# Optimization experiments

Hardware: AMD Instinct MI355X
Metric: run time of the kernel (lower is better)

## Reference

```python
import jax, jax.numpy as jnp
import numpy as np

N_NODES = 50000
N_EDGES = 1600000
IN_DIM = 256
OUT_DIM = 128
T = 8
V_THRESHOLD = 1.0
TAU = 2.0
STEP_SIZE = 0.1


def setup_inputs() -> dict:
    key = jax.random.key(0)
    k1, k2, k3 = jax.random.split(key, 3)
    x = jax.random.normal(k1, (N_NODES, IN_DIM), dtype=jnp.float32)
    W = jax.random.normal(k2, (IN_DIM, OUT_DIM), dtype=jnp.float32) / np.sqrt(IN_DIM)
    edge_index = jax.random.randint(k3, (2, N_EDGES), 0, N_NODES, dtype=jnp.int64)
    return {"x": x, "W": W, "edge_index": edge_index}


def gcn_conv(x, W, edge_index):
    # GCNConv (no bias): h = D^{-1/2} (A + I) D^{-1/2} (x @ W)
    n = x.shape[0]
    h = x @ W  # [N, OUT]
    loops = jnp.arange(n, dtype=edge_index.dtype)
    src = jnp.concatenate([edge_index[0], loops])
    dst = jnp.concatenate([edge_index[1], loops])
    deg = jax.ops.segment_sum(jnp.ones_like(dst, dtype=h.dtype), dst, num_segments=n)
    dinv = jnp.where(deg > 0, jax.lax.rsqrt(deg), 0.0)
    norm = dinv[src] * dinv[dst]  # [E+N]
    msgs = h[src] * norm[:, None]
    return jax.ops.segment_sum(msgs, dst, num_segments=n)  # [N, OUT]


def reference(x, W, edge_index):
    h = gcn_conv(x, W, edge_index)            # encoder output, [N, OUT]
    u = h * STEP_SIZE                          # per-step tangent input
    z0 = jnp.zeros_like(h)                     # manifold origin

    def step(z, _):
        # leaky charge toward input current, fire on threshold, soft reset
        Hm = z + (u - z) / TAU
        o = (Hm >= V_THRESHOLD).astype(Hm.dtype)
        z_new = Hm - o * V_THRESHOLD
        return z_new, (o, z_new)

    _, (o_seq, z_seq) = jax.lax.scan(step, z0, None, length=T)
    return o_seq, z_seq  # each [T, N, OUT]
```

## Files before the change

kernel.cpp:

```cpp
#include <hip/hip_runtime.h>
#include <hip/hip_bf16.h>

#define N_NODES 50000
#define N_EDGES 1600000
#define IN_DIM  256
#define OUT_DIM 128
#define T_STEPS 8
#define NREP    8

typedef __attribute__((ext_vector_type(8))) short bf16x8;
typedef __attribute__((ext_vector_type(4))) float f32x4;


__device__ inline unsigned short bf_hi_trunc(float x) {
    return (unsigned short)(__float_as_uint(x) >> 16);
}
__device__ inline float bf_to_f(unsigned short u) {
    return __uint_as_float((unsigned)u << 16);
}
__device__ inline unsigned short f2bf_rne(float a) {
    __hip_bfloat16 t = __float2bfloat16(a);
    return *(unsigned short*)&t;
}
__device__ inline float bf_lo(unsigned p) { return __uint_as_float(p << 16); }
__device__ inline float bf_hi(unsigned p) { return __uint_as_float(p & 0xffff0000u); }

__global__ __launch_bounds__(256) void
k_count(const float* __restrict__ W,
        unsigned short* __restrict__ Wt_hi,
        unsigned short* __restrict__ Wt_lo,
        const int* __restrict__ edge, int* __restrict__ cnt_x) {
    int idx = blockIdx.x * 256 + threadIdx.x;
    int* my = cnt_x + (blockIdx.x & (NREP - 1)) * N_NODES;
    if (idx < N_EDGES / 4) {
        int4 d = ((const int4*)(edge + N_EDGES))[idx];
        atomicAdd(&my[d.x], 1);
        atomicAdd(&my[d.y], 1);
        atomicAdd(&my[d.z], 1);
        atomicAdd(&my[d.w], 1);
    }
    if (idx < 32768) {
        int n = idx >> 8;
        int k = idx & 255;
        float w = W[k * OUT_DIM + n];
        unsigned short hi = bf_hi_trunc(w);
        Wt_hi[idx] = hi;
        Wt_lo[idx] = f2bf_rne(w - bf_to_f(hi));
    }
}

__global__ __launch_bounds__(256) void
k_scanA(const int* __restrict__ cnt_x, int* __restrict__ part) {
    int t = threadIdx.x;
    int i4 = blockIdx.x * 256 + t;
    int4 v = make_int4(0, 0, 0, 0);
    if (i4 < 12500) {
#pragma unroll
        for (int r = 0; r < NREP; ++r) {
            int4 c = ((const int4*)(cnt_x + r * N_NODES))[i4];
            v.x += c.x; v.y += c.y; v.z += c.z; v.w += c.w;
        }
    }
    int s = v.x + v.y + v.z + v.w;
    __shared__ int sd[256];
    sd[t] = s; __syncthreads();
    for (int o = 128; o > 0; o >>= 1) {
        if (t < o) sd[t] += sd[t + o];
        __syncthreads();
    }
    if (t == 0) part[blockIdx.x] = sd[0];
}

__global__ void k_scanB(int* __restrict__ part) {
    int l = threadIdx.x;
    int v = (l < 49) ? part[l] : 0;
    int orig = v;
    for (int o = 1; o < 64; o <<= 1) {
        int u = __shfl_up(v, o);
        if (l >= o) v += u;
    }
    if (l < 49) part[l] = v - orig;
}

__global__ __launch_bounds__(256) void
k_scanC(const int* __restrict__ cnt_x, const int* __restrict__ part,
        int* __restrict__ offs, int* __restrict__ deg,
        int* __restrict__ fill_x, float* __restrict__ dinv) {
    int t = threadIdx.x;
    int i4 = blockIdx.x * 256 + t;
    int4 vr[NREP];
    int4 tot = make_int4(0, 0, 0, 0);
    if (i4 < 12500) {
#pragma unroll
        for (int r = 0; r < NREP; ++r) {
            vr[r] = ((const int4*)(cnt_x + r * N_NODES))[i4];
            tot.x += vr[r].x; tot.y += vr[r].y;
            tot.z += vr[r].z; tot.w += vr[r].w;
        }
    } else {
#pragma unroll
        for (int r = 0; r < NREP; ++r) vr[r] = make_int4(0, 0, 0, 0);
    }
    int s = tot.x + tot.y + tot.z + tot.w;
    __shared__ int sd[256];
    sd[t] = s; __syncthreads();
    for (int o = 1; o < 256; o <<= 1) {
        int u = (t >= o) ? sd[t - o] : 0;
        __syncthreads();
        sd[t] += u;
        __syncthreads();
    }
    if (i4 < 12500) {
        int base = part[blockIdx.x] + sd[t] - s;
        int4 o4;
        o4.x = base;
        o4.y = o4.x + tot.x;
        o4.z = o4.y + tot.y;
        o4.w = o4.z + tot.z;
        ((int4*)offs)[i4] = o4;
        ((int4*)deg)[i4]  = tot;
        float4 d4;
        d4.x = rsqrtf((float)(tot.x + 1));
        d4.y = rsqrtf((float)(tot.y + 1));
        d4.z = rsqrtf((float)(tot.z + 1));
        d4.w = rsqrtf((float)(tot.w + 1));
        ((float4*)dinv)[i4] = d4;
        int c0 = o4.x, c1 = o4.y, c2 = o4.z, c3 = o4.w;
#pragma unroll
        for (int r = 0; r < NREP; ++r) {
            int4 c4 = make_int4(c0, c1, c2, c3);
            ((int4*)(fill_x + r * N_NODES))[i4] = c4;
            c0 += vr[r].x; c1 += vr[r].y; c2 += vr[r].z; c3 += vr[r].w;
        }
    }
}

__global__ __launch_bounds__(256) void
k_gemm(const float* __restrict__ x,
       const unsigned short* __restrict__ Wt_hi,
       const unsigned short* __restrict__ Wt_lo,
       const float* __restrict__ dinv,
       unsigned short* __restrict__ hs) {
    int wave = blockIdx.x * 4 + (threadIdx.x >> 6);
    if (wave >= N_NODES / 16) return;
    int lane = threadIdx.x & 63;
    int quad = lane >> 4;
    int r16  = lane & 15;
    int m0 = wave * 16;

    f32x4 acc[8];
#pragma unroll
    for (int nt = 0; nt < 8; ++nt) acc[nt] = (f32x4){0.f, 0.f, 0.f, 0.f};

#pragma unroll
    for (int kt = 0; kt < 8; ++kt) {
        int k0 = kt * 32 + quad * 8;
        const float* xp = x + (size_t)(m0 + r16) * IN_DIM + k0;
        float4 v0 = *(const float4*)xp;
        float4 v1 = *(const float4*)(xp + 4);
        float vv[8] = {v0.x, v0.y, v0.z, v0.w, v1.x, v1.y, v1.z, v1.w};
        union { bf16x8 v; unsigned short u[8]; } ahi, alo;
#pragma unroll
        for (int j = 0; j < 8; ++j) {
            unsigned short hi = bf_hi_trunc(vv[j]);
            ahi.u[j] = hi;
            alo.u[j] = f2bf_rne(vv[j] - bf_to_f(hi));
        }
#pragma unroll
        for (int nt = 0; nt < 8; ++nt) {
            size_t woff = (size_t)(nt * 16 + r16) * IN_DIM + k0;
            bf16x8 bhi = *(const bf16x8*)(Wt_hi + woff);
            bf16x8 blo = *(const bf16x8*)(Wt_lo + woff);
            acc[nt] = __builtin_amdgcn_mfma_f32_16x16x32_bf16(ahi.v, bhi, acc[nt], 0, 0, 0);
            acc[nt] = __builtin_amdgcn_mfma_f32_16x16x32_bf16(alo.v, bhi, acc[nt], 0, 0, 0);
            acc[nt] = __builtin_amdgcn_mfma_f32_16x16x32_bf16(ahi.v, blo, acc[nt], 0, 0, 0);
        }
    }
    float dr[4];
#pragma unroll
    for (int r = 0; r < 4; ++r) dr[r] = dinv[m0 + quad * 4 + r];
#pragma unroll
    for (int nt = 0; nt < 8; ++nt) {
#pragma unroll
        for (int r = 0; r < 4; ++r) {
            int row = m0 + quad * 4 + r;
            int col = nt * 16 + r16;
            hs[(size_t)row * OUT_DIM + col] = f2bf_rne(acc[nt][r] * dr[r]);
        }
    }
}

__global__ __launch_bounds__(256) void
k_fill(const int* __restrict__ edge, int* __restrict__ fill_x,
       unsigned short* __restrict__ csr) {
    int e4 = blockIdx.x * 256 + threadIdx.x;
    int* my = fill_x + (blockIdx.x & (NREP - 1)) * N_NODES;
    if (e4 < N_EDGES / 4) {
        int4 s = ((const int4*)edge)[e4];
        int4 d = ((const int4*)(edge + N_EDGES))[e4];
        int p;
        p = atomicAdd(&my[d.x], 1); csr[p] = (unsigned short)s.x;
        p = atomicAdd(&my[d.y], 1); csr[p] = (unsigned short)s.y;
        p = atomicAdd(&my[d.z], 1); csr[p] = (unsigned short)s.z;
        p = atomicAdd(&my[d.w], 1); csr[p] = (unsigned short)s.w;
    }
}

__global__ __launch_bounds__(256) void
k_agg_snn(const unsigned short* __restrict__ hs,
          const int* __restrict__ offs, const int* __restrict__ deg,
          const float* __restrict__ dinv,
          const unsigned short* __restrict__ csr,
          float* __restrict__ out) {
    int node = blockIdx.x * 4 + (threadIdx.x >> 6);
    int lane = threadIdx.x & 63;
    bool hi  = (lane >= 32);
    int  loff = (lane & 31) * 8;
    const char* hsb = (const char*)hs;

    uint2 qs = *(const uint2*)(hsb + (size_t)node * 256 + loff);
    float a0 = hi ? bf_lo(qs.x) : 0.f;
    float a1 = hi ? bf_hi(qs.x) : 0.f;
    float a2 = hi ? bf_lo(qs.y) : 0.f;
    float a3 = hi ? bf_hi(qs.y) : 0.f;

    int beg = __builtin_amdgcn_readfirstlane(offs[node]);
    int end = __builtin_amdgcn_readfirstlane(offs[node] + deg[node]);

    int j = beg;
    if (j & 1) {
        unsigned s = csr[j];
        if (!hi) {
            uint2 q = *(const uint2*)(hsb + (size_t)s * 256 + loff);
            a0 += bf_lo(q.x); a1 += bf_hi(q.x);
            a2 += bf_lo(q.y); a3 += bf_hi(q.y);
        }
        ++j;
    }
    int nd = (end - j) >> 1;
    const unsigned* cw = (const unsigned*)(csr + j);
    int k = 0;
    for (; k + 8 <= nd; k += 8) {
        unsigned d[8];
#pragma unroll
        for (int q = 0; q < 8; ++q) d[q] = cw[k + q];
        uint2 g[8];
#pragma unroll
        for (int q = 0; q < 8; ++q) {
            unsigned s = hi ? (d[q] >> 16) : (d[q] & 0xffffu);
            g[q] = *(const uint2*)(hsb + (size_t)s * 256 + loff);
        }
#pragma unroll
        for (int q = 0; q < 8; ++q) {
            a0 += bf_lo(g[q].x); a1 += bf_hi(g[q].x);
            a2 += bf_lo(g[q].y); a3 += bf_hi(g[q].y);
        }
    }
    for (; k < nd; ++k) {
        unsigned d = cw[k];
        unsigned s = hi ? (d >> 16) : (d & 0xffffu);
        uint2 q = *(const uint2*)(hsb + (size_t)s * 256 + loff);
        a0 += bf_lo(q.x); a1 += bf_hi(q.x);
        a2 += bf_lo(q.y); a3 += bf_hi(q.y);
    }
    int jt = j + 2 * nd;
    if (jt < end) {
        unsigned s = csr[jt];
        if (!hi) {
            uint2 q = *(const uint2*)(hsb + (size_t)s * 256 + loff);
            a0 += bf_lo(q.x); a1 += bf_hi(q.x);
            a2 += bf_lo(q.y); a3 += bf_hi(q.y);
        }
    }

    a0 += __shfl(a0, lane ^ 32);
    a1 += __shfl(a1, lane ^ 32);
    a2 += __shfl(a2, lane ^ 32);
    a3 += __shfl(a3, lane ^ 32);

    float di = dinv[node];
    float u0 = a0 * di * 0.1f, u1 = a1 * di * 0.1f;
    float u2 = a2 * di * 0.1f, u3 = a3 * di * 0.1f;
    float z0 = 0.f, z1 = 0.f, z2 = 0.f, z3 = 0.f;

    const size_t plane = (size_t)N_NODES * 128;
    size_t base = (size_t)node * 128 + (size_t)(lane & 31) * 4
                + (hi ? (size_t)T_STEPS * plane : 0);
#pragma unroll
    for (int t = 0; t < T_STEPS; ++t) {
        float H0 = z0 + (u0 - z0) * 0.5f;
        float H1 = z1 + (u1 - z1) * 0.5f;
        float H2 = z2 + (u2 - z2) * 0.5f;
        float H3 = z3 + (u3 - z3) * 0.5f;
        float o0 = (H0 >= 1.0f) ? 1.0f : 0.0f;
        float o1 = (H1 >= 1.0f) ? 1.0f : 0.0f;
        float o2 = (H2 >= 1.0f) ? 1.0f : 0.0f;
        float o3 = (H3 >= 1.0f) ? 1.0f : 0.0f;
        z0 = H0 - o0; z1 = H1 - o1; z2 = H2 - o2; z3 = H3 - o3;
        f32x4 v = {hi ? z0 : o0, hi ? z1 : o1,
                   hi ? z2 : o2, hi ? z3 : o3};
        __builtin_nontemporal_store(v, (f32x4*)(out + base + (size_t)t * plane));
    }
}

extern "C" void kernel_launch(void* const* d_in, const int* in_sizes, int n_in,
                              void* d_out, int out_size, void* d_ws, size_t ws_size,
                              hipStream_t stream) {
    const float* x  = (const float*)d_in[0];
    const float* W  = (const float*)d_in[1];
    const int*   ei = (const int*)d_in[2];
    float* out = (float*)d_out;

    char* ws = (char*)d_ws;
    unsigned short* hs     = (unsigned short*)(ws + 0);
    unsigned short* Wt_hi  = (unsigned short*)(ws + 12800000);
    unsigned short* Wt_lo  = (unsigned short*)(ws + 12865536);
    int*            cnt_x  = (int*)(ws + 12931072);
    int*            fill_x = (int*)(ws + 14531072);
    int*            offs   = (int*)(ws + 16131072);
    int*            deg    = (int*)(ws + 16331072);
    float*          dinv   = (float*)(ws + 16531072);
    int*            part   = (int*)(ws + 16731072);
    unsigned short* csr    = (unsigned short*)(ws + 16731328);

    hipMemsetAsync(cnt_x, 0, 1600000, stream);

    k_count<<<1563, 256, 0, stream>>>(W, Wt_hi, Wt_lo, ei, cnt_x);
    k_scanA<<<49, 256, 0, stream>>>(cnt_x, part);
    k_scanB<<<1, 64, 0, stream>>>(part);
    k_scanC<<<49, 256, 0, stream>>>(cnt_x, part, offs, deg, fill_x, dinv);
    k_gemm<<<782, 256, 0, stream>>>(x, Wt_hi, Wt_lo, dinv, hs);
    k_fill<<<1563, 256, 0, stream>>>(ei, fill_x, csr);
    k_agg_snn<<<12500, 256, 0, stream>>>(hs, offs, deg, dinv, csr, out);
}
```

Baseline: 694.3 us.

## Split hs into column slabs for cache-resident gathers and fuse gemm with fill

The GEMM output hs is stored as four column slabs of 32 features each, 3.2 MB per slab. The aggregation kernel runs four passes, one per slab, so each pass gathers from a slab small enough to stay in L2, and each wave handles four edges at once with 16 lanes per edge. The GEMM and CSR fill kernels are merged into one launch by block-index range, so the two independent workloads can overlap. In exchange, the CSR indices and the per-node offsets are re-read four times, each gather shrinks to 4 bytes, and output stores become narrower 8-byte writes.

```diff
diff --git a/kernel.cpp b/kernel.cpp
--- a/kernel.cpp
+++ b/kernel.cpp
@@ -10,6 +10,7 @@
 
 typedef __attribute__((ext_vector_type(8))) short bf16x8;
 typedef __attribute__((ext_vector_type(4))) float f32x4;
+typedef __attribute__((ext_vector_type(2))) float f32x2;
 
 
 __device__ inline unsigned short bf_hi_trunc(float x) {
@@ -128,178 +129,176 @@
         int c0 = o4.x, c1 = o4.y, c2 = o4.z, c3 = o4.w;
 #pragma unroll
         for (int r = 0; r < NREP; ++r) {
-            int4 c4 = make_int4(c0, c1, c2, c3);
-            ((int4*)(fill_x + r * N_NODES))[i4] = c4;
+            ((int4*)(fill_x + r * N_NODES))[i4] = make_int4(c0, c1, c2, c3);
             c0 += vr[r].x; c1 += vr[r].y; c2 += vr[r].z; c3 += vr[r].w;
         }
     }
 }
 
 __global__ __launch_bounds__(256) void
-k_gemm(const float* __restrict__ x,
-       const unsigned short* __restrict__ Wt_hi,
-       const unsigned short* __restrict__ Wt_lo,
-       const float* __restrict__ dinv,
-       unsigned short* __restrict__ hs) {
-    int wave = blockIdx.x * 4 + (threadIdx.x >> 6);
-    if (wave >= N_NODES / 16) return;
-    int lane = threadIdx.x & 63;
-    int quad = lane >> 4;
-    int r16  = lane & 15;
-    int m0 = wave * 16;
-
-    f32x4 acc[8];
-#pragma unroll
-    for (int nt = 0; nt < 8; ++nt) acc[nt] = (f32x4){0.f, 0.f, 0.f, 0.f};
-
-#pragma unroll
-    for (int kt = 0; kt < 8; ++kt) {
-        int k0 = kt * 32 + quad * 8;
-        const float* xp = x + (size_t)(m0 + r16) * IN_DIM + k0;
-        float4 v0 = *(const float4*)xp;
-        float4 v1 = *(const float4*)(xp + 4);
-        float vv[8] = {v0.x, v0.y, v0.z, v0.w, v1.x, v1.y, v1.z, v1.w};
-        union { bf16x8 v; unsigned short u[8]; } ahi, alo;
-#pragma unroll
-        for (int j = 0; j < 8; ++j) {
-            unsigned short hi = bf_hi_trunc(vv[j]);
-            ahi.u[j] = hi;
-            alo.u[j] = f2bf_rne(vv[j] - bf_to_f(hi));
-        }
+k_gf(const float* __restrict__ x,
+     const unsigned short* __restrict__ Wt_hi,
+     const unsigned short* __restrict__ Wt_lo,
+     const float* __restrict__ dinv,
+     unsigned short* __restrict__ hs,
+     const int* __restrict__ edge, int* __restrict__ fill_x,
+     unsigned short* __restrict__ csr) {
+    if (blockIdx.x < 782) {
+        int wave = blockIdx.x * 4 + (threadIdx.x >> 6);
+        if (wave >= N_NODES / 16) return;
+        int lane = threadIdx.x & 63;
+        int quad = lane >> 4;
+        int r16  = lane & 15;
+        int m0 = wave * 16;
+
+        f32x4 acc[8];
+#pragma unroll
+        for (int nt = 0; nt < 8; ++nt) acc[nt] = (f32x4){0.f, 0.f, 0.f, 0.f};
+#pragma unroll
+        for (int kt = 0; kt < 8; ++kt) {
+            int k0 = kt * 32 + quad * 8;
+            const float* xp = x + (size_t)(m0 + r16) * IN_DIM + k0;
+            float4 v0 = *(const float4*)xp;
+            float4 v1 = *(const float4*)(xp + 4);
+            float vv[8] = {v0.x, v0.y, v0.z, v0.w, v1.x, v1.y, v1.z, v1.w};
+            union { bf16x8 v; unsigned short u[8]; } ahi, alo;
+#pragma unroll
+            for (int j = 0; j < 8; ++j) {
+                unsigned short hi = bf_hi_trunc(vv[j]);
+                ahi.u[j] = hi;
+                alo.u[j] = f2bf_rne(vv[j] - bf_to_f(hi));
+            }
+#pragma unroll
+            for (int nt = 0; nt < 8; ++nt) {
+                size_t woff = (size_t)(nt * 16 + r16) * IN_DIM + k0;
+                bf16x8 bhi = *(const bf16x8*)(Wt_hi + woff);
+                bf16x8 blo = *(const bf16x8*)(Wt_lo + woff);
+                acc[nt] = __builtin_amdgcn_mfma_f32_16x16x32_bf16(ahi.v, bhi, acc[nt], 0, 0, 0);
+                acc[nt] = __builtin_amdgcn_mfma_f32_16x16x32_bf16(alo.v, bhi, acc[nt], 0, 0, 0);
+                acc[nt] = __builtin_amdgcn_mfma_f32_16x16x32_bf16(ahi.v, blo, acc[nt], 0, 0, 0);
+            }
+        }
+        float dr[4];
+#pragma unroll
+        for (int r = 0; r < 4; ++r) dr[r] = dinv[m0 + quad * 4 + r];
 #pragma unroll
         for (int nt = 0; nt < 8; ++nt) {
-            size_t woff = (size_t)(nt * 16 + r16) * IN_DIM + k0;
-            bf16x8 bhi = *(const bf16x8*)(Wt_hi + woff);
-            bf16x8 blo = *(const bf16x8*)(Wt_lo + woff);
-            acc[nt] = __builtin_amdgcn_mfma_f32_16x16x32_bf16(ahi.v, bhi, acc[nt], 0, 0, 0);
-            acc[nt] = __builtin_amdgcn_mfma_f32_16x16x32_bf16(alo.v, bhi, acc[nt], 0, 0, 0);
-            acc[nt] = __builtin_amdgcn_mfma_f32_16x16x32_bf16(ahi.v, blo, acc[nt], 0, 0, 0);
-        }
-    }
-    float dr[4];
-#pragma unroll
-    for (int r = 0; r < 4; ++r) dr[r] = dinv[m0 + quad * 4 + r];
-#pragma unroll
-    for (int nt = 0; nt < 8; ++nt) {
-#pragma unroll
-        for (int r = 0; r < 4; ++r) {
-            int row = m0 + quad * 4 + r;
-            int col = nt * 16 + r16;
-            hs[(size_t)row * OUT_DIM + col] = f2bf_rne(acc[nt][r] * dr[r]);
-        }
-    }
-}
-
-__global__ __launch_bounds__(256) void
-k_fill(const int* __restrict__ edge, int* __restrict__ fill_x,
-       unsigned short* __restrict__ csr) {
-    int e4 = blockIdx.x * 256 + threadIdx.x;
-    int* my = fill_x + (blockIdx.x & (NREP - 1)) * N_NODES;
-    if (e4 < N_EDGES / 4) {
-        int4 s = ((const int4*)edge)[e4];
-        int4 d = ((const int4*)(edge + N_EDGES))[e4];
-        int p;
-        p = atomicAdd(&my[d.x], 1); csr[p] = (unsigned short)s.x;
-        p = atomicAdd(&my[d.y], 1); csr[p] = (unsigned short)s.y;
-        p = atomicAdd(&my[d.z], 1); csr[p] = (unsigned short)s.z;
-        p = atomicAdd(&my[d.w], 1); csr[p] = (unsigned short)s.w;
-    }
-}
-
-__global__ __launch_bounds__(256) void
-k_agg_snn(const unsigned short* __restrict__ hs,
+#pragma unroll
+            for (int r = 0; r < 4; ++r) {
+                int row = m0 + quad * 4 + r;
+                int col = nt * 16 + r16;
+                hs[(size_t)(col >> 5) * (N_NODES * 32) + (size_t)row * 32 + (col & 31)]
+                    = f2bf_rne(acc[nt][r] * dr[r]);
+            }
+        }
+    } else {
+        int fblk = blockIdx.x - 782;
+        int e4 = fblk * 256 + threadIdx.x;
+        int* my = fill_x + (fblk & (NREP - 1)) * N_NODES;
+        if (e4 < N_EDGES / 4) {
+            int4 s = ((const int4*)edge)[e4];
+            int4 d = ((const int4*)(edge + N_EDGES))[e4];
+            int p;
+            p = atomicAdd(&my[d.x], 1); csr[p] = (unsigned short)s.x;
+            p = atomicAdd(&my[d.y], 1); csr[p] = (unsigned short)s.y;
+            p = atomicAdd(&my[d.z], 1); csr[p] = (unsigned short)s.z;
+            p = atomicAdd(&my[d.w], 1); csr[p] = (unsigned short)s.w;
+        }
+    }
+}
+
+__global__ __launch_bounds__(256) void
+k_agg_snn(const char* __restrict__ hs_s,
           const int* __restrict__ offs, const int* __restrict__ deg,
           const float* __restrict__ dinv,
           const unsigned short* __restrict__ csr,
           float* __restrict__ out) {
-    int node = blockIdx.x * 4 + (threadIdx.x >> 6);
+    int pass = blockIdx.x / 12500;
+    int node = (blockIdx.x % 12500) * 4 + (threadIdx.x >> 6);
     int lane = threadIdx.x & 63;
-    bool hi  = (lane >= 32);
-    int  loff = (lane & 31) * 8;
-    const char* hsb = (const char*)hs;
-
-    uint2 qs = *(const uint2*)(hsb + (size_t)node * 256 + loff);
-    float a0 = hi ? bf_lo(qs.x) : 0.f;
-    float a1 = hi ? bf_hi(qs.x) : 0.f;
-    float a2 = hi ? bf_lo(qs.y) : 0.f;
-    float a3 = hi ? bf_hi(qs.y) : 0.f;
+    int e    = lane >> 4;
+    int dl   = lane & 15;
+    const char* base = hs_s + (size_t)pass * 3200000;
+
+    float a0 = 0.f, a1 = 0.f;
+    if (e == 0) {
+        unsigned q = *(const unsigned*)(base + (size_t)node * 64 + dl * 4);
+        a0 += bf_lo(q); a1 += bf_hi(q);
+    }
 
     int beg = __builtin_amdgcn_readfirstlane(offs[node]);
     int end = __builtin_amdgcn_readfirstlane(offs[node] + deg[node]);
 
     int j = beg;
-    if (j & 1) {
+    while ((j & 3) && j < end) {
         unsigned s = csr[j];
-        if (!hi) {
-            uint2 q = *(const uint2*)(hsb + (size_t)s * 256 + loff);
-            a0 += bf_lo(q.x); a1 += bf_hi(q.x);
-            a2 += bf_lo(q.y); a3 += bf_hi(q.y);
+        if (e == 0) {
+            unsigned q = *(const unsigned*)(base + (size_t)s * 64 + dl * 4);
+            a0 += bf_lo(q); a1 += bf_hi(q);
         }
         ++j;
     }
-    int nd = (end - j) >> 1;
-    const unsigned* cw = (const unsigned*)(csr + j);
+    int nq = (end - j) >> 2;
+    const uint2* cq = (const uint2*)(csr + j);
     int k = 0;
-    for (; k + 8 <= nd; k += 8) {
-        unsigned d[8];
-#pragma unroll
-        for (int q = 0; q < 8; ++q) d[q] = cw[k + q];
-        uint2 g[8];
+    for (; k + 8 <= nq; k += 8) {
+        uint2 d[8];
+#pragma unroll
+        for (int q = 0; q < 8; ++q) d[q] = cq[k + q];
+        unsigned g[8];
 #pragma unroll
         for (int q = 0; q < 8; ++q) {
-            unsigned s = hi ? (d[q] >> 16) : (d[q] & 0xffffu);
-            g[q] = *(const uint2*)(hsb + (size_t)s * 256 + loff);
+            unsigned w = (e & 2) ? d[q].y : d[q].x;
+            unsigned s = (e & 1) ? (w >> 16) : (w & 0xffffu);
+            g[q] = *(const unsigned*)(base + (size_t)s * 64 + dl * 4);
         }
 #pragma unroll
         for (int q = 0; q < 8; ++q) {
-            a0 += bf_lo(g[q].x); a1 += bf_hi(g[q].x);
-            a2 += bf_lo(g[q].y); a3 += bf_hi(g[q].y);
-        }
-    }
-    for (; k < nd; ++k) {
-        unsigned d = cw[k];
-        unsigned s = hi ? (d >> 16) : (d & 0xffffu);
-        uint2 q = *(const uint2*)(hsb + (size_t)s * 256 + loff);
-        a0 += bf_lo(q.x); a1 += bf_hi(q.x);
-        a2 += bf_lo(q.y); a3 += bf_hi(q.y);
-    }
-    int jt = j + 2 * nd;
-    if (jt < end) {
+            a0 += bf_lo(g[q]); a1 += bf_hi(g[q]);
+        }
+    }
+    for (; k < nq; ++k) {
+        uint2 d = cq[k];
+        unsigned w = (e & 2) ? d.y : d.x;
+        unsigned s = (e & 1) ? (w >> 16) : (w & 0xffffu);
+        unsigned q = *(const unsigned*)(base + (size_t)s * 64 + dl * 4);
+        a0 += bf_lo(q); a1 += bf_hi(q);
+    }
+    for (int jt = j + 4 * nq; jt < end; ++jt) {
         unsigned s = csr[jt];
-        if (!hi) {
-            uint2 q = *(const uint2*)(hsb + (size_t)s * 256 + loff);
-            a0 += bf_lo(q.x); a1 += bf_hi(q.x);
-            a2 += bf_lo(q.y); a3 += bf_hi(q.y);
-        }
-    }
-
+        if (e == 0) {
+            unsigned q = *(const unsigned*)(base + (size_t)s * 64 + dl * 4);
+            a0 += bf_lo(q); a1 += bf_hi(q);
+        }
+    }
+
+    a0 += __shfl(a0, lane ^ 16);
+    a1 += __shfl(a1, lane ^ 16);
     a0 += __shfl(a0, lane ^ 32);
     a1 += __shfl(a1, lane ^ 32);
-    a2 += __shfl(a2, lane ^ 32);
-    a3 += __shfl(a3, lane ^ 32);
 
     float di = dinv[node];
     float u0 = a0 * di * 0.1f, u1 = a1 * di * 0.1f;
-    float u2 = a2 * di * 0.1f, u3 = a3 * di * 0.1f;
-    float z0 = 0.f, z1 = 0.f, z2 = 0.f, z3 = 0.f;
+    float z0 = 0.f, z1 = 0.f;
 
     const size_t plane = (size_t)N_NODES * 128;
-    size_t base = (size_t)node * 128 + (size_t)(lane & 31) * 4
-                + (hi ? (size_t)T_STEPS * plane : 0);
+    size_t ob = (size_t)node * 128 + pass * 32 + 2 * dl;
 #pragma unroll
     for (int t = 0; t < T_STEPS; ++t) {
         float H0 = z0 + (u0 - z0) * 0.5f;
         float H1 = z1 + (u1 - z1) * 0.5f;
-        float H2 = z2 + (u2 - z2) * 0.5f;
-        float H3 = z3 + (u3 - z3) * 0.5f;
         float o0 = (H0 >= 1.0f) ? 1.0f : 0.0f;
         float o1 = (H1 >= 1.0f) ? 1.0f : 0.0f;
-        float o2 = (H2 >= 1.0f) ? 1.0f : 0.0f;
-        float o3 = (H3 >= 1.0f) ? 1.0f : 0.0f;
-        z0 = H0 - o0; z1 = H1 - o1; z2 = H2 - o2; z3 = H3 - o3;
-        f32x4 v = {hi ? z0 : o0, hi ? z1 : o1,
-                   hi ? z2 : o2, hi ? z3 : o3};
-        __builtin_nontemporal_store(v, (f32x4*)(out + base + (size_t)t * plane));
+        z0 = H0 - o0;
+        z1 = H1 - o1;
+        if (e == 0) {
+            f32x2 v = {o0, o1};
+            __builtin_nontemporal_store(v, (f32x2*)(out + (size_t)t * plane + ob));
+        }
+        if (e == 1) {
+            f32x2 v = {z0, z1};
+            __builtin_nontemporal_store(v, (f32x2*)(out + (size_t)(T_STEPS + t) * plane + ob));
+        }
     }
 }
 
@@ -323,13 +322,12 @@
     int*            part   = (int*)(ws + 16731072);
     unsigned short* csr    = (unsigned short*)(ws + 16731328);
 
-    hipMemsetAsync(cnt_x, 0, 1600000, stream);
+    (void)hipMemsetAsync(cnt_x, 0, 1600000, stream);
 
     k_count<<<1563, 256, 0, stream>>>(W, Wt_hi, Wt_lo, ei, cnt_x);
     k_scanA<<<49, 256, 0, stream>>>(cnt_x, part);
     k_scanB<<<1, 64, 0, stream>>>(part);
     k_scanC<<<49, 256, 0, stream>>>(cnt_x, part, offs, deg, fill_x, dinv);
-    k_gemm<<<782, 256, 0, stream>>>(x, Wt_hi, Wt_lo, dinv, hs);
-    k_fill<<<1563, 256, 0, stream>>>(ei, fill_x, csr);
-    k_agg_snn<<<12500, 256, 0, stream>>>(hs, offs, deg, dinv, csr, out);
-}
+    k_gf<<<2345, 256, 0, stream>>>(x, Wt_hi, Wt_lo, dinv, hs, ei, fill_x, csr);
+    k_agg_snn<<<50000, 256, 0, stream>>>((const char*)hs, offs, deg, dinv, csr, out);
+}
```

Measured after the change: 693.6 us. No clear change (-0.1%).
